# Kernel optimization log

Hardware: AMD Instinct MI355X
Metric: run time of the kernel (lower is better)

Reference implementation:

```python
import jax, jax.numpy as jnp
import numpy as np

BUCKET_SIZE = 64  # must divide seq_len


def setup_inputs() -> dict:
    key = jax.random.key(0)
    k1, k2, k3, k4 = jax.random.split(key, 4)
    B, S, D = 4, 4096, 1024
    query = jax.random.normal(k1, (B, S, D), dtype=jnp.float32)
    key_t = jax.random.normal(k2, (B, S, D), dtype=jnp.float32)
    value = jax.random.normal(k3, (B, S, D), dtype=jnp.float32)
    # random hashing hyperplanes: [B, D, bucket_size // 2]
    R = jax.random.normal(k4, (B, D, BUCKET_SIZE // 2), dtype=jnp.float32)
    return {"query": query, "key": key_t, "value": value, "R": R}


def reference(query, key, value, R):
    B, S, D = query.shape
    # random projection: [B, S, bucket_size // 2]
    xR = jnp.einsum("bsd,bdr->bsr", query, R)
    # mirror trick -> [B, S, bucket_size]
    concat_xR = jnp.concatenate([xR, -xR], axis=-1)
    buckets = jnp.argmax(concat_xR, axis=-1)          # [B, S] int
    sticker = jnp.argsort(buckets, axis=-1)            # token permutation into buckets
    undo_sort = jnp.argsort(sticker, axis=-1)          # computed in original (unused)
    # batched gather (tf.gather batch_dims=1, axis=1)
    sorted_query = jnp.take_along_axis(query, sticker[..., None], axis=1)
    sorted_value = jnp.take_along_axis(value, sticker[..., None], axis=1)
    # tf.split(x, bucket_size, 1) then stack(axis=1) == reshape to chunks
    chunked_query = sorted_query.reshape(B, BUCKET_SIZE, S // BUCKET_SIZE, D)
    chunked_value = sorted_value.reshape(B, BUCKET_SIZE, S // BUCKET_SIZE, D)
    del undo_sort, chunked_query, chunked_value  # dead code in original; module returns sticker
    return sticker
```

## Files before the change

### kernel.cpp

```cpp
#include <hip/hip_runtime.h>


#define B_DIM 4
#define S_LEN 4096
#define D_DIM 1024
#define NRR 32
#define NBK 64
#define TMK 32
#define NC32 (S_LEN / TMK)
#define KB 256
#define NTILE (D_DIM / KB)

__global__ void __launch_bounds__(512) __attribute__((amdgpu_waves_per_eu(2, 4)))
k1_buckets(const float* __restrict__ Q, const float* __restrict__ R,
           int* __restrict__ buckets, int* __restrict__ hist)
{
    __shared__ float lds[16384];
    __shared__ int cnt[NBK];

    const int t = threadIdx.x;
    const int b = blockIdx.x >> 7;
    const int c32 = blockIdx.x & (NC32 - 1);

    const int lane = t & 63;
    const int w = t >> 6;
    const int rq = lane & 7;
    const int tg = (lane >> 3) & 3;
    const int kh = lane >> 5;
    const int kbase = w * 32 + kh * 16;

    const float* Qg = Q + ((size_t)b * S_LEN + c32 * TMK) * D_DIM;
    const float* Rg = R + (size_t)b * D_DIM * NRR;

    float4 acc[8];
#pragma unroll
    for (int j = 0; j < 8; ++j) acc[j] = make_float4(0.f, 0.f, 0.f, 0.f);

    for (int tile = 0; tile < NTILE; ++tile) {
        if (tile) __syncthreads();
        {
            const float* Qt = Qg + tile * KB;
#pragma unroll
            for (int i = 0; i < 4; ++i) {
                const int f = t + 512 * i;
                const int row = f >> 6;
                const int q = f & 63;
                const float4 v = *(const float4*)(Qt + (size_t)row * D_DIM + q * 4);
                *(float4*)&lds[row * KB + ((q ^ (row >> 3)) << 2)] = v;
            }
            const float* Rt = Rg + (size_t)tile * KB * NRR;
#pragma unroll
            for (int i = 0; i < 4; ++i) {
                const int f = t + 512 * i;
                const float4 v = *(const float4*)(Rt + f * 4);
                *(float4*)&lds[8192 + f * 4] = v;
            }
        }
        __syncthreads();
#pragma unroll
        for (int kk4 = 0; kk4 < 4; ++kk4) {
            const int k0 = kbase + kk4 * 4;
            const float4 rv0 = *(const float4*)&lds[8192 + (k0 + 0) * NRR + rq * 4];
            const float4 rv1 = *(const float4*)&lds[8192 + (k0 + 1) * NRR + rq * 4];
            const float4 rv2 = *(const float4*)&lds[8192 + (k0 + 2) * NRR + rq * 4];
            const float4 rv3 = *(const float4*)&lds[8192 + (k0 + 3) * NRR + rq * 4];
            const int qq = (k0 >> 2) ^ tg;
#pragma unroll
            for (int j = 0; j < 8; ++j) {
                const int tok = tg * 8 + j;
                const float4 q = *(const float4*)&lds[tok * KB + (qq << 2)];
                acc[j].x = fmaf(q.x, rv0.x, acc[j].x);
                acc[j].y = fmaf(q.x, rv0.y, acc[j].y);
                acc[j].z = fmaf(q.x, rv0.z, acc[j].z);
                acc[j].w = fmaf(q.x, rv0.w, acc[j].w);
                acc[j].x = fmaf(q.y, rv1.x, acc[j].x);
                acc[j].y = fmaf(q.y, rv1.y, acc[j].y);
                acc[j].z = fmaf(q.y, rv1.z, acc[j].z);
                acc[j].w = fmaf(q.y, rv1.w, acc[j].w);
                acc[j].x = fmaf(q.z, rv2.x, acc[j].x);
                acc[j].y = fmaf(q.z, rv2.y, acc[j].y);
                acc[j].z = fmaf(q.z, rv2.z, acc[j].z);
                acc[j].w = fmaf(q.z, rv2.w, acc[j].w);
                acc[j].x = fmaf(q.w, rv3.x, acc[j].x);
                acc[j].y = fmaf(q.w, rv3.y, acc[j].y);
                acc[j].z = fmaf(q.w, rv3.z, acc[j].z);
                acc[j].w = fmaf(q.w, rv3.w, acc[j].w);
            }
        }
    }

#pragma unroll
    for (int j = 0; j < 8; ++j) {
        acc[j].x += __shfl_xor(acc[j].x, 32, 64);
        acc[j].y += __shfl_xor(acc[j].y, 32, 64);
        acc[j].z += __shfl_xor(acc[j].z, 32, 64);
        acc[j].w += __shfl_xor(acc[j].w, 32, 64);
    }
    if (t < NBK) cnt[t] = 0;
    __syncthreads();

    if (kh == 0) {
        float* red = &lds[8192 + w * (TMK * NRR)];
#pragma unroll
        for (int j = 0; j < 8; ++j)
            *(float4*)&red[(tg * 8 + j) * NRR + rq * 4] = acc[j];
    }
    __syncthreads();

#pragma unroll
    for (int it = 0; it < 2; ++it) {
        const int p = t + it * 512;
        const int tok = p >> 5, r = p & 31;
        float s = 0.f;
#pragma unroll
        for (int ww = 0; ww < 8; ++ww)
            s += lds[8192 + ww * (TMK * NRR) + tok * NRR + r];
        lds[tok * 33 + r] = s;
    }
    __syncthreads();

    if (t < TMK) {
        float m1 = lds[t * 33 + 0]; int i1 = 0;
        float m2 = m1;              int i2 = 0;
#pragma unroll
        for (int r = 1; r < NRR; ++r) {
            const float v = lds[t * 33 + r];
            if (v > m1) { m1 = v; i1 = r; }
            if (v < m2) { m2 = v; i2 = r; }
        }
        const int bk = (m1 >= -m2) ? i1 : (NRR + i2);
        buckets[(size_t)b * S_LEN + c32 * TMK + t] = bk;
        atomicAdd(&cnt[bk], 1);
    }
    __syncthreads();
    if (t < NBK) hist[((size_t)b * NC32 + c32) * NBK + t] = cnt[t];
}

__global__ __launch_bounds__(256) void k2_scan(
    const int* __restrict__ hist, int* __restrict__ chunkOffset)
{
    const int t = threadIdx.x;
    const int b = t >> 6;
    const int bk = t & 63;
    const int lane = t & 63;

    int total = 0;
    for (int c = 0; c < NC32; ++c)
        total += hist[((size_t)b * NC32 + c) * NBK + bk];

    int incl = total;
#pragma unroll
    for (int off = 1; off < 64; off <<= 1) {
        int n = __shfl_up(incl, off, 64);
        if (lane >= off) incl += n;
    }
    int run = incl - total;

    for (int c = 0; c < NC32; ++c) {
        int h = hist[((size_t)b * NC32 + c) * NBK + bk];
        chunkOffset[((size_t)b * NC32 + c) * NBK + bk] = run;
        run += h;
    }
}

__global__ __launch_bounds__(256) void k3_scatter(
    const int* __restrict__ buckets, const int* __restrict__ chunkOffset,
    int* __restrict__ out)
{
    const int gid = blockIdx.x * 256 + threadIdx.x;
    const int b = gid >> 12;
    const int s = gid & (S_LEN - 1);
    const int chunk = s >> 5;
    const int lane = threadIdx.x & 63;

    const int bk = buckets[gid];

    unsigned long long m = ~0ull;
#pragma unroll
    for (int i = 0; i < 6; ++i) {
        unsigned long long bi = __ballot((bk >> i) & 1);
        m &= ((bk >> i) & 1) ? bi : ~bi;
    }
    const unsigned int m32 = (unsigned int)(m >> (lane & 32));
    const int rank = __popc(m32 & ((1u << (lane & 31)) - 1u));

    const int pos = chunkOffset[((size_t)b * NC32 + chunk) * NBK + bk] + rank;
    out[(size_t)b * S_LEN + pos] = s;
}

extern "C" void kernel_launch(void* const* d_in, const int* in_sizes, int n_in,
                              void* d_out, int out_size, void* d_ws, size_t ws_size,
                              hipStream_t stream) {
    const float* Q = (const float*)d_in[0];
    const float* R = (const float*)d_in[3];

    int* buckets     = (int*)d_ws;
    int* hist        = buckets + B_DIM * S_LEN;
    int* chunkOffset = hist + B_DIM * NC32 * NBK;

    k1_buckets<<<B_DIM * NC32, 512, 0, stream>>>(Q, R, buckets, hist);
    k2_scan   <<<1,            256, 0, stream>>>(hist, chunkOffset);
    k3_scatter<<<(B_DIM * S_LEN) / 256, 256, 0, stream>>>(buckets, chunkOffset, (int*)d_out);
}
```

Baseline: 44.88 us.

## Restructure projection GEMM with double-buffered LDS tiles and register prefetch

Rewrites the bucket projection kernel to use 256-thread blocks, 128-wide K tiles with double-buffered shared memory, and global loads for the next tile issued before computing the current one. Each thread now holds a larger 16-token by 8-projection accumulator tile with swizzled R layout to avoid bank conflicts, followed by a pairwise shuffle and 16-slice LDS reduction. The goal is to hide global memory latency of the Q stream and to increase FMA work per LDS read, in exchange for much higher register pressure and lower thread count per block.

```diff
diff --git a/kernel.cpp b/kernel.cpp
--- a/kernel.cpp
+++ b/kernel.cpp
@@ -8,123 +8,190 @@
 #define NBK 64
 #define TMK 32
 #define NC32 (S_LEN / TMK)
-#define KB 256
-#define NTILE (D_DIM / KB)
-
-__global__ void __launch_bounds__(512) __attribute__((amdgpu_waves_per_eu(2, 4)))
-k1_buckets(const float* __restrict__ Q, const float* __restrict__ R,
-           int* __restrict__ buckets, int* __restrict__ hist)
+#define TILE_K 128
+#define NT (D_DIM / TILE_K)
+
+__global__ __launch_bounds__(256) __attribute__((amdgpu_waves_per_eu(2, 2)))
+void k1_buckets(const float* __restrict__ Q, const float* __restrict__ R,
+                int* __restrict__ buckets, int* __restrict__ hist)
 {
-    __shared__ float lds[16384];
+    __shared__ float4 smem4[4096];
+    __shared__ float xs[TMK * 33];
     __shared__ int cnt[NBK];
 
     const int t = threadIdx.x;
     const int b = blockIdx.x >> 7;
-    const int c32 = blockIdx.x & (NC32 - 1);
+    const int c32 = blockIdx.x & 127;
 
     const int lane = t & 63;
     const int w = t >> 6;
-    const int rq = lane & 7;
-    const int tg = (lane >> 3) & 3;
-    const int kh = lane >> 5;
-    const int kbase = w * 32 + kh * 16;
-
-    const float* Qg = Q + ((size_t)b * S_LEN + c32 * TMK) * D_DIM;
-    const float* Rg = R + (size_t)b * D_DIM * NRR;
-
-    float4 acc[8];
-#pragma unroll
-    for (int j = 0; j < 8; ++j) acc[j] = make_float4(0.f, 0.f, 0.f, 0.f);
-
-    for (int tile = 0; tile < NTILE; ++tile) {
-        if (tile) __syncthreads();
-        {
-            const float* Qt = Qg + tile * KB;
-#pragma unroll
-            for (int i = 0; i < 4; ++i) {
-                const int f = t + 512 * i;
-                const int row = f >> 6;
-                const int q = f & 63;
-                const float4 v = *(const float4*)(Qt + (size_t)row * D_DIM + q * 4);
-                *(float4*)&lds[row * KB + ((q ^ (row >> 3)) << 2)] = v;
+    const int tok_t = lane >> 5;
+    const int r_t = (lane >> 3) & 3;
+    const int kl = lane & 7;
+    const int kappa = w * 8 + kl;
+
+    const float4* Qg4 = (const float4*)(Q + ((size_t)b * S_LEN + c32 * TMK) * D_DIM);
+    const float4* Rg4 = (const float4*)(R + (size_t)b * D_DIM * NRR);
+
+    const float4* qsrc[4];
+    const float4* rsrc[4];
+#pragma unroll
+    for (int i = 0; i < 4; ++i) {
+        const int s = t + 256 * i;
+        qsrc[i] = Qg4 + (size_t)(s >> 5) * 256 + (s & 31);
+        const int K = s >> 3;
+        rsrc[i] = Rg4 + (size_t)K * 8 + ((s & 7) ^ ((K >> 3) & 3));
+    }
+    const int rswap = (t >> 5) & 1;
+
+    float2 acc[16][4];
+#pragma unroll
+    for (int j = 0; j < 16; ++j)
+#pragma unroll
+        for (int p = 0; p < 4; ++p) acc[j][p] = make_float2(0.f, 0.f);
+
+    const int qoff = tok_t * 512 + kappa;
+    int rboff[4];
+#pragma unroll
+    for (int p = 0; p < 4; ++p) rboff[p] = kappa * 64 + ((r_t * 4 + p) ^ kl);
+
+#define LOADS(TILE)                                                           \
+    float4 qld[4], rld[4];                                                    \
+    _Pragma("unroll")                                                         \
+    for (int i = 0; i < 4; ++i) {                                             \
+        qld[i] = qsrc[i][(TILE) * 32];                                        \
+        float4 v = rsrc[i][(TILE) * 1024];                                    \
+        rld[i] = rswap ? make_float4(v.z, v.w, v.x, v.y) : v;                 \
+    }
+
+#define WRITES(DST)                                                           \
+    {                                                                         \
+        float4* qb = smem4 + (DST) * 1024;                                    \
+        float4* rb = smem4 + 2048 + (DST) * 1024;                             \
+        _Pragma("unroll")                                                     \
+        for (int i = 0; i < 4; ++i) {                                         \
+            qb[t + 256 * i] = qld[i];                                         \
+            rb[t + 256 * i] = rld[i];                                         \
+        }                                                                     \
+    }
+
+    {
+        LOADS(0)
+        WRITES(0)
+    }
+    __syncthreads();
+
+    for (int tau = 0; tau < NT; ++tau) {
+        const int cur = tau & 1;
+        if (tau + 1 < NT) {
+            LOADS(tau + 1)
+            {
+                const float4* qb = smem4 + cur * 1024;
+                const float2* rb = (const float2*)(smem4 + 2048 + cur * 1024);
+                float2 rv[4][4];
+#pragma unroll
+                for (int kk = 0; kk < 4; ++kk)
+#pragma unroll
+                    for (int p = 0; p < 4; ++p)
+                        rv[kk][p] = rb[rboff[p] + kk * 16];
+#pragma unroll
+                for (int tq = 0; tq < 4; ++tq) {
+                    float4 qv[4];
+#pragma unroll
+                    for (int jj = 0; jj < 4; ++jj)
+                        qv[jj] = qb[qoff + (tq * 4 + jj) * 32];
+#pragma unroll
+                    for (int jj = 0; jj < 4; ++jj)
+#pragma unroll
+                        for (int kk = 0; kk < 4; ++kk) {
+                            const float s = kk == 0 ? qv[jj].x : kk == 1 ? qv[jj].y
+                                          : kk == 2 ? qv[jj].z : qv[jj].w;
+#pragma unroll
+                            for (int p = 0; p < 4; ++p) {
+                                acc[tq * 4 + jj][p].x = fmaf(s, rv[kk][p].x, acc[tq * 4 + jj][p].x);
+                                acc[tq * 4 + jj][p].y = fmaf(s, rv[kk][p].y, acc[tq * 4 + jj][p].y);
+                            }
+                        }
+                }
             }
-            const float* Rt = Rg + (size_t)tile * KB * NRR;
-#pragma unroll
-            for (int i = 0; i < 4; ++i) {
-                const int f = t + 512 * i;
-                const float4 v = *(const float4*)(Rt + f * 4);
-                *(float4*)&lds[8192 + f * 4] = v;
+            WRITES(cur ^ 1)
+        } else {
+            const float4* qb = smem4 + cur * 1024;
+            const float2* rb = (const float2*)(smem4 + 2048 + cur * 1024);
+            float2 rv[4][4];
+#pragma unroll
+            for (int kk = 0; kk < 4; ++kk)
+#pragma unroll
+                for (int p = 0; p < 4; ++p)
+                    rv[kk][p] = rb[rboff[p] + kk * 16];
+#pragma unroll
+            for (int tq = 0; tq < 4; ++tq) {
+                float4 qv[4];
+#pragma unroll
+                for (int jj = 0; jj < 4; ++jj)
+                    qv[jj] = qb[qoff + (tq * 4 + jj) * 32];
+#pragma unroll
+                for (int jj = 0; jj < 4; ++jj)
+#pragma unroll
+                    for (int kk = 0; kk < 4; ++kk) {
+                        const float s = kk == 0 ? qv[jj].x : kk == 1 ? qv[jj].y
+                                      : kk == 2 ? qv[jj].z : qv[jj].w;
+#pragma unroll
+                        for (int p = 0; p < 4; ++p) {
+                            acc[tq * 4 + jj][p].x = fmaf(s, rv[kk][p].x, acc[tq * 4 + jj][p].x);
+                            acc[tq * 4 + jj][p].y = fmaf(s, rv[kk][p].y, acc[tq * 4 + jj][p].y);
+                        }
+                    }
             }
         }
         __syncthreads();
-#pragma unroll
-        for (int kk4 = 0; kk4 < 4; ++kk4) {
-            const int k0 = kbase + kk4 * 4;
-            const float4 rv0 = *(const float4*)&lds[8192 + (k0 + 0) * NRR + rq * 4];
-            const float4 rv1 = *(const float4*)&lds[8192 + (k0 + 1) * NRR + rq * 4];
-            const float4 rv2 = *(const float4*)&lds[8192 + (k0 + 2) * NRR + rq * 4];
-            const float4 rv3 = *(const float4*)&lds[8192 + (k0 + 3) * NRR + rq * 4];
-            const int qq = (k0 >> 2) ^ tg;
-#pragma unroll
-            for (int j = 0; j < 8; ++j) {
-                const int tok = tg * 8 + j;
-                const float4 q = *(const float4*)&lds[tok * KB + (qq << 2)];
-                acc[j].x = fmaf(q.x, rv0.x, acc[j].x);
-                acc[j].y = fmaf(q.x, rv0.y, acc[j].y);
-                acc[j].z = fmaf(q.x, rv0.z, acc[j].z);
-                acc[j].w = fmaf(q.x, rv0.w, acc[j].w);
-                acc[j].x = fmaf(q.y, rv1.x, acc[j].x);
-                acc[j].y = fmaf(q.y, rv1.y, acc[j].y);
-                acc[j].z = fmaf(q.y, rv1.z, acc[j].z);
-                acc[j].w = fmaf(q.y, rv1.w, acc[j].w);
-                acc[j].x = fmaf(q.z, rv2.x, acc[j].x);
-                acc[j].y = fmaf(q.z, rv2.y, acc[j].y);
-                acc[j].z = fmaf(q.z, rv2.z, acc[j].z);
-                acc[j].w = fmaf(q.z, rv2.w, acc[j].w);
-                acc[j].x = fmaf(q.w, rv3.x, acc[j].x);
-                acc[j].y = fmaf(q.w, rv3.y, acc[j].y);
-                acc[j].z = fmaf(q.w, rv3.z, acc[j].z);
-                acc[j].w = fmaf(q.w, rv3.w, acc[j].w);
-            }
-        }
-    }
-
-#pragma unroll
-    for (int j = 0; j < 8; ++j) {
-        acc[j].x += __shfl_xor(acc[j].x, 32, 64);
-        acc[j].y += __shfl_xor(acc[j].y, 32, 64);
-        acc[j].z += __shfl_xor(acc[j].z, 32, 64);
-        acc[j].w += __shfl_xor(acc[j].w, 32, 64);
+    }
+#undef LOADS
+#undef WRITES
+
+#pragma unroll
+    for (int j = 0; j < 16; ++j)
+#pragma unroll
+        for (int p = 0; p < 4; ++p) {
+            acc[j][p].x += __shfl_xor(acc[j][p].x, 1, 64);
+            acc[j][p].y += __shfl_xor(acc[j][p].y, 1, 64);
+        }
+
+    if ((kl & 1) == 0) {
+        const int slice = w * 4 + (kl >> 1);
+#pragma unroll
+        for (int j = 0; j < 16; ++j) {
+            const int tok = tok_t * 16 + j;
+            smem4[slice * 256 + tok * 8 + r_t * 2 + 0] =
+                make_float4(acc[j][0].x, acc[j][0].y, acc[j][1].x, acc[j][1].y);
+            smem4[slice * 256 + tok * 8 + r_t * 2 + 1] =
+                make_float4(acc[j][2].x, acc[j][2].y, acc[j][3].x, acc[j][3].y);
+        }
     }
     if (t < NBK) cnt[t] = 0;
     __syncthreads();
 
-    if (kh == 0) {
-        float* red = &lds[8192 + w * (TMK * NRR)];
-#pragma unroll
-        for (int j = 0; j < 8; ++j)
-            *(float4*)&red[(tg * 8 + j) * NRR + rq * 4] = acc[j];
-    }
-    __syncthreads();
-
-#pragma unroll
-    for (int it = 0; it < 2; ++it) {
-        const int p = t + it * 512;
-        const int tok = p >> 5, r = p & 31;
-        float s = 0.f;
-#pragma unroll
-        for (int ww = 0; ww < 8; ++ww)
-            s += lds[8192 + ww * (TMK * NRR) + tok * NRR + r];
-        lds[tok * 33 + r] = s;
+    {
+        float4 s = smem4[t];
+#pragma unroll
+        for (int sl = 1; sl < 16; ++sl) {
+            const float4 v = smem4[sl * 256 + t];
+            s.x += v.x; s.y += v.y; s.z += v.z; s.w += v.w;
+        }
+        const int tok = t >> 3, rq = t & 7;
+        xs[tok * 33 + rq * 4 + 0] = s.x;
+        xs[tok * 33 + rq * 4 + 1] = s.y;
+        xs[tok * 33 + rq * 4 + 2] = s.z;
+        xs[tok * 33 + rq * 4 + 3] = s.w;
     }
     __syncthreads();
 
     if (t < TMK) {
-        float m1 = lds[t * 33 + 0]; int i1 = 0;
-        float m2 = m1;              int i2 = 0;
+        float m1 = xs[t * 33 + 0]; int i1 = 0;
+        float m2 = m1;             int i2 = 0;
 #pragma unroll
         for (int r = 1; r < NRR; ++r) {
-            const float v = lds[t * 33 + r];
+            const float v = xs[t * 33 + r];
             if (v > m1) { m1 = v; i1 = r; }
             if (v < m2) { m2 = v; i2 = r; }
         }
@@ -198,7 +265,7 @@
     int* hist        = buckets + B_DIM * S_LEN;
     int* chunkOffset = hist + B_DIM * NC32 * NBK;
 
-    k1_buckets<<<B_DIM * NC32, 512, 0, stream>>>(Q, R, buckets, hist);
+    k1_buckets<<<B_DIM * NC32, 256, 0, stream>>>(Q, R, buckets, hist);
     k2_scan   <<<1,            256, 0, stream>>>(hist, chunkOffset);
     k3_scatter<<<(B_DIM * S_LEN) / 256, 256, 0, stream>>>(buckets, chunkOffset, (int*)d_out);
 }
```

After: 156.8 us. 249% more time.

## Double-buffer projection tiles with async global-to-LDS loads and re-map threads

Applied to the files above, without the earlier changes.

Rewrites the projection kernel to stream Q and R tiles straight into LDS with global_load_lds, using two buffers so the next tile's load overlaps the current tile's FMAs, paced by explicit vmcnt waits. Tiles shrink to 128 columns over eight iterations, with new XOR swizzles and a thread mapping in which each lane holds 8 tokens by 8 projections. The partial-sum reduction switches from a shuffle across half-waves to shuffles across 4 lanes. The goal is to hide global load latency and cut register staging. The price is a dependence on hand-written waitcnt counts and on swizzle arithmetic being correct.

```diff
diff --git a/kernel.cpp b/kernel.cpp
--- a/kernel.cpp
+++ b/kernel.cpp
@@ -8,123 +8,156 @@
 #define NBK 64
 #define TMK 32
 #define NC32 (S_LEN / TMK)
-#define KB 256
-#define NTILE (D_DIM / KB)
-
-__global__ void __launch_bounds__(512) __attribute__((amdgpu_waves_per_eu(2, 4)))
-k1_buckets(const float* __restrict__ Q, const float* __restrict__ R,
-           int* __restrict__ buckets, int* __restrict__ hist)
+#define NT 8
+
+typedef const __attribute__((address_space(1))) void* gas_t;
+typedef __attribute__((address_space(3))) void* las_t;
+
+__global__ __launch_bounds__(512, 4)
+void k1_buckets(const float* __restrict__ Q, const float* __restrict__ R,
+                int* __restrict__ buckets, int* __restrict__ hist)
 {
-    __shared__ float lds[16384];
+    __shared__ float4 smem4[4096];
+    __shared__ float xs[TMK * 33];
     __shared__ int cnt[NBK];
 
     const int t = threadIdx.x;
     const int b = blockIdx.x >> 7;
-    const int c32 = blockIdx.x & (NC32 - 1);
-
+    const int c32 = blockIdx.x & 127;
+
+    const int w = t >> 6;
     const int lane = t & 63;
-    const int w = t >> 6;
-    const int rq = lane & 7;
-    const int tg = (lane >> 3) & 3;
-    const int kh = lane >> 5;
-    const int kbase = w * 32 + kh * 16;
-
-    const float* Qg = Q + ((size_t)b * S_LEN + c32 * TMK) * D_DIM;
-    const float* Rg = R + (size_t)b * D_DIM * NRR;
-
-    float4 acc[8];
-#pragma unroll
-    for (int j = 0; j < 8; ++j) acc[j] = make_float4(0.f, 0.f, 0.f, 0.f);
-
-    for (int tile = 0; tile < NTILE; ++tile) {
-        if (tile) __syncthreads();
-        {
-            const float* Qt = Qg + tile * KB;
-#pragma unroll
-            for (int i = 0; i < 4; ++i) {
-                const int f = t + 512 * i;
-                const int row = f >> 6;
-                const int q = f & 63;
-                const float4 v = *(const float4*)(Qt + (size_t)row * D_DIM + q * 4);
-                *(float4*)&lds[row * KB + ((q ^ (row >> 3)) << 2)] = v;
-            }
-            const float* Rt = Rg + (size_t)tile * KB * NRR;
-#pragma unroll
-            for (int i = 0; i < 4; ++i) {
-                const int f = t + 512 * i;
-                const float4 v = *(const float4*)(Rt + f * 4);
-                *(float4*)&lds[8192 + f * 4] = v;
-            }
+    const int tok_t = lane >> 4;
+    const int r_t = (lane >> 2) & 3;
+    const int kl = lane & 3;
+    const int kq = w * 4 + kl;
+    const int qx = kq ^ ((tok_t & 1) << 2);
+
+    const float4* Qg4 = (const float4*)(Q + ((size_t)b * S_LEN + c32 * TMK) * D_DIM);
+    const float4* Rg4 = (const float4*)(R + (size_t)b * D_DIM * NRR);
+
+    const float4* qsrc[2];
+    const float4* rsrc[2];
+#pragma unroll
+    for (int i = 0; i < 2; ++i) {
+        const int f = i * 512 + t;
+        const int tok = f >> 5, s = f & 31;
+        const int swz = (tok & 7) ^ (((tok >> 3) & 1) << 2);
+        qsrc[i] = Qg4 + (size_t)tok * 256 + (s ^ swz);
+        const int kloc = f >> 3, rq = f & 7;
+        rsrc[i] = Rg4 + (size_t)kloc * 8 + (rq ^ ((kloc >> 2) & 3));
+    }
+    const int dwb = t & ~63;
+
+#define ISSUE(TILE, D)                                                        \
+    {                                                                         \
+        _Pragma("unroll")                                                     \
+        for (int i = 0; i < 2; ++i) {                                         \
+            __builtin_amdgcn_global_load_lds(                                 \
+                (gas_t)(qsrc[i] + (TILE) * 32),                               \
+                (las_t)&smem4[(D) * 1024 + i * 512 + dwb], 16, 0, 0);         \
+            __builtin_amdgcn_global_load_lds(                                 \
+                (gas_t)(rsrc[i] + (size_t)(TILE) * 1024),                     \
+                (las_t)&smem4[2048 + (D) * 1024 + i * 512 + dwb], 16, 0, 0);  \
+        }                                                                     \
+    }
+
+#define COMPUTE(D)                                                            \
+    {                                                                         \
+        const float4* qb = smem4 + (D) * 1024;                                \
+        const float4* rb = smem4 + 2048 + (D) * 1024;                         \
+        float4 rv[4][2];                                                      \
+        _Pragma("unroll")                                                     \
+        for (int kk = 0; kk < 4; ++kk)                                        \
+            _Pragma("unroll")                                                 \
+            for (int p = 0; p < 2; ++p)                                       \
+                rv[kk][p] = rb[kq * 32 + kk * 8 + ((r_t * 2 + p) ^ kl)];      \
+        _Pragma("unroll")                                                     \
+        for (int j = 0; j < 8; ++j) {                                         \
+            const float4 qv = qb[tok_t * 256 + j * 32 + (qx ^ j)];            \
+            _Pragma("unroll")                                                 \
+            for (int kk = 0; kk < 4; ++kk) {                                  \
+                const float s = kk == 0 ? qv.x : kk == 1 ? qv.y               \
+                              : kk == 2 ? qv.z : qv.w;                        \
+                _Pragma("unroll")                                             \
+                for (int p = 0; p < 2; ++p) {                                 \
+                    acc[j][p].x = fmaf(s, rv[kk][p].x, acc[j][p].x);          \
+                    acc[j][p].y = fmaf(s, rv[kk][p].y, acc[j][p].y);          \
+                    acc[j][p].z = fmaf(s, rv[kk][p].z, acc[j][p].z);          \
+                    acc[j][p].w = fmaf(s, rv[kk][p].w, acc[j][p].w);          \
+                }                                                             \
+            }                                                                 \
+        }                                                                     \
+    }
+
+    float4 acc[8][2];
+#pragma unroll
+    for (int j = 0; j < 8; ++j) {
+        acc[j][0] = make_float4(0.f, 0.f, 0.f, 0.f);
+        acc[j][1] = make_float4(0.f, 0.f, 0.f, 0.f);
+    }
+
+    ISSUE(0, 0)
+    for (int tau = 0; tau < NT; ++tau) {
+        if (tau + 1 < NT) {
+            ISSUE(tau + 1, (tau + 1) & 1)
+            asm volatile("s_waitcnt vmcnt(4)" ::: "memory");
+        } else {
+            asm volatile("s_waitcnt vmcnt(0)" ::: "memory");
         }
         __syncthreads();
-#pragma unroll
-        for (int kk4 = 0; kk4 < 4; ++kk4) {
-            const int k0 = kbase + kk4 * 4;
-            const float4 rv0 = *(const float4*)&lds[8192 + (k0 + 0) * NRR + rq * 4];
-            const float4 rv1 = *(const float4*)&lds[8192 + (k0 + 1) * NRR + rq * 4];
-            const float4 rv2 = *(const float4*)&lds[8192 + (k0 + 2) * NRR + rq * 4];
-            const float4 rv3 = *(const float4*)&lds[8192 + (k0 + 3) * NRR + rq * 4];
-            const int qq = (k0 >> 2) ^ tg;
-#pragma unroll
-            for (int j = 0; j < 8; ++j) {
-                const int tok = tg * 8 + j;
-                const float4 q = *(const float4*)&lds[tok * KB + (qq << 2)];
-                acc[j].x = fmaf(q.x, rv0.x, acc[j].x);
-                acc[j].y = fmaf(q.x, rv0.y, acc[j].y);
-                acc[j].z = fmaf(q.x, rv0.z, acc[j].z);
-                acc[j].w = fmaf(q.x, rv0.w, acc[j].w);
-                acc[j].x = fmaf(q.y, rv1.x, acc[j].x);
-                acc[j].y = fmaf(q.y, rv1.y, acc[j].y);
-                acc[j].z = fmaf(q.y, rv1.z, acc[j].z);
-                acc[j].w = fmaf(q.y, rv1.w, acc[j].w);
-                acc[j].x = fmaf(q.z, rv2.x, acc[j].x);
-                acc[j].y = fmaf(q.z, rv2.y, acc[j].y);
-                acc[j].z = fmaf(q.z, rv2.z, acc[j].z);
-                acc[j].w = fmaf(q.z, rv2.w, acc[j].w);
-                acc[j].x = fmaf(q.w, rv3.x, acc[j].x);
-                acc[j].y = fmaf(q.w, rv3.y, acc[j].y);
-                acc[j].z = fmaf(q.w, rv3.z, acc[j].z);
-                acc[j].w = fmaf(q.w, rv3.w, acc[j].w);
-            }
-        }
-    }
-
-#pragma unroll
-    for (int j = 0; j < 8; ++j) {
-        acc[j].x += __shfl_xor(acc[j].x, 32, 64);
-        acc[j].y += __shfl_xor(acc[j].y, 32, 64);
-        acc[j].z += __shfl_xor(acc[j].z, 32, 64);
-        acc[j].w += __shfl_xor(acc[j].w, 32, 64);
-    }
+        COMPUTE(tau & 1)
+        __syncthreads();
+    }
+#undef ISSUE
+#undef COMPUTE
+
+#pragma unroll
+    for (int j = 0; j < 8; ++j)
+#pragma unroll
+        for (int p = 0; p < 2; ++p) {
+            acc[j][p].x += __shfl_xor(acc[j][p].x, 1, 64);
+            acc[j][p].y += __shfl_xor(acc[j][p].y, 1, 64);
+            acc[j][p].z += __shfl_xor(acc[j][p].z, 1, 64);
+            acc[j][p].w += __shfl_xor(acc[j][p].w, 1, 64);
+            acc[j][p].x += __shfl_xor(acc[j][p].x, 2, 64);
+            acc[j][p].y += __shfl_xor(acc[j][p].y, 2, 64);
+            acc[j][p].z += __shfl_xor(acc[j][p].z, 2, 64);
+            acc[j][p].w += __shfl_xor(acc[j][p].w, 2, 64);
+        }
+
     if (t < NBK) cnt[t] = 0;
+    if (kl == 0) {
+#pragma unroll
+        for (int j = 0; j < 8; ++j) {
+            const int tok = tok_t * 8 + j;
+            smem4[w * 256 + tok * 8 + r_t * 2 + 0] = acc[j][0];
+            smem4[w * 256 + tok * 8 + r_t * 2 + 1] = acc[j][1];
+        }
+    }
     __syncthreads();
 
-    if (kh == 0) {
-        float* red = &lds[8192 + w * (TMK * NRR)];
-#pragma unroll
-        for (int j = 0; j < 8; ++j)
-            *(float4*)&red[(tg * 8 + j) * NRR + rq * 4] = acc[j];
+    if (t < 256) {
+        float4 s = smem4[t];
+#pragma unroll
+        for (int ww = 1; ww < 8; ++ww) {
+            const float4 v = smem4[ww * 256 + t];
+            s.x += v.x; s.y += v.y; s.z += v.z; s.w += v.w;
+        }
+        const int tok = t >> 3, r2 = t & 7;
+        xs[tok * 33 + r2 * 4 + 0] = s.x;
+        xs[tok * 33 + r2 * 4 + 1] = s.y;
+        xs[tok * 33 + r2 * 4 + 2] = s.z;
+        xs[tok * 33 + r2 * 4 + 3] = s.w;
     }
     __syncthreads();
 
-#pragma unroll
-    for (int it = 0; it < 2; ++it) {
-        const int p = t + it * 512;
-        const int tok = p >> 5, r = p & 31;
-        float s = 0.f;
-#pragma unroll
-        for (int ww = 0; ww < 8; ++ww)
-            s += lds[8192 + ww * (TMK * NRR) + tok * NRR + r];
-        lds[tok * 33 + r] = s;
-    }
-    __syncthreads();
-
     if (t < TMK) {
-        float m1 = lds[t * 33 + 0]; int i1 = 0;
-        float m2 = m1;              int i2 = 0;
+        float m1 = xs[t * 33 + 0]; int i1 = 0;
+        float m2 = m1;             int i2 = 0;
 #pragma unroll
         for (int r = 1; r < NRR; ++r) {
-            const float v = lds[t * 33 + r];
+            const float v = xs[t * 33 + r];
             if (v > m1) { m1 = v; i1 = r; }
             if (v < m2) { m2 = v; i2 = r; }
         }
```

After: 42.72 us. -4.8%, faster.
